# Kernel optimization log

Measured on AMD Instinct MI355X. Metric: run time of the kernel, lower is better.

The kernel has to match this reference:

```python
import jax, jax.numpy as jnp
import numpy as np

K = 10

def _lrelu(v):
    return jax.nn.leaky_relu(v, negative_slope=0.2)

def _knn_idx(x, k):
    # x: [B, C, N]; returns indices of k nearest neighbors [B, N, k]
    xx = jnp.sum(x * x, axis=1, keepdims=True)          # [B,1,N]
    inner = -2.0 * jnp.einsum('bcn,bcm->bnm', x, x)     # [B,N,N]
    pd = -xx - inner - jnp.swapaxes(xx, 1, 2)           # -squared distance [B,N,N]
    _, idx = jax.lax.top_k(pd, k)
    return idx

def _graph_feature(x, k):
    # x: [B, C, N] -> edge features [B, 2C, N, k]
    idx = _knn_idx(x, k)                                # [B,N,k]
    xt = jnp.swapaxes(x, 1, 2)                          # [B,N,C]
    feat = jax.vmap(lambda xb, ib: xb[ib])(xt, idx)     # [B,N,k,C] gather
    center = xt[:, :, None, :]                          # [B,N,1,C]
    f = jnp.concatenate([feat - center,
                         jnp.broadcast_to(center, feat.shape)], axis=-1)  # [B,N,k,2C]
    return jnp.transpose(f, (0, 3, 1, 2))               # [B,2C,N,k]

def _edge_block(x, W, k):
    # conv2d 1x1 (no bias) + LeakyReLU + max over neighbors
    g = _graph_feature(x, k)                            # [B,2C,N,k]
    h = _lrelu(jnp.einsum('oc,bcnk->bonk', W, g))
    return jnp.max(h, axis=-1)                          # [B,O,N]

def setup_inputs() -> dict:
    key = jax.random.key(0)
    ks = jax.random.split(key, 9)
    def w(k_, *shape):
        fan_in = shape[-1]
        return jax.random.normal(k_, shape, dtype=jnp.float32) / np.sqrt(fan_in)
    return {
        'x':  jax.random.normal(ks[0], (8, 3, 2048), dtype=jnp.float32),
        'W1': w(ks[1], 64, 6),
        'W2': w(ks[2], 64, 128),
        'W3': w(ks[3], 128, 128),
        'W4': w(ks[4], 256, 256),
        'W5': w(ks[5], 512, 512),
        'L1': w(ks[6], 512, 1024),
        'L2': w(ks[7], 256, 512),
        'b2': jnp.zeros((256,), dtype=jnp.float32),
    }

def reference(x, W1, W2, W3, W4, W5, L1, L2, b2):
    x1 = _edge_block(x,  W1, K)   # [B,64,N]
    x2 = _edge_block(x1, W2, K)   # [B,64,N]
    x3 = _edge_block(x2, W3, K)   # [B,128,N]
    x4 = _edge_block(x3, W4, K)   # [B,256,N]
    h = jnp.concatenate([x1, x2, x3, x4], axis=1)        # [B,512,N]
    h = _lrelu(jnp.einsum('oc,bcn->bon', W5, h))         # [B,512,N]
    hmax = jnp.max(h, axis=-1)                           # [B,512]
    havg = jnp.mean(h, axis=-1)                          # [B,512]
    f = jnp.concatenate([hmax, havg], axis=1)            # [B,1024]
    f = _lrelu(f @ L1.T)                                 # [B,512]
    out = _lrelu(f @ L2.T + b2)                          # [B,256]
    return out
```

## Files before the change

kernel.cpp:

```cpp
#include <hip/hip_runtime.h>
#include <cstdint>
#include <cstddef>

constexpr int B_ = 8;
constexpr int N_ = 2048;
constexpr int K_ = 10;

typedef __attribute__((ext_vector_type(8))) short bf16x8;
typedef __attribute__((ext_vector_type(4))) float f32x4;

__device__ __forceinline__ float lrelu(float v) { return fmaxf(v, 0.2f * v); }

__device__ __forceinline__ short f2bf(float f) {
    uint32_t u = __builtin_bit_cast(uint32_t, f);
    u += 0x7fff + ((u >> 16) & 1);
    return (short)(u >> 16);
}

__global__ void k_transpose(const float* __restrict__ x, float* __restrict__ xt) {
    int i = blockIdx.x * 256 + threadIdx.x;
    if (i >= B_ * N_) return;
    int b = i / N_, n = i % N_;
#pragma unroll
    for (int c = 0; c < 3; ++c)
        xt[(size_t)i * 3 + c] = x[((size_t)b * 3 + c) * N_ + n];
}

__global__ void k_cvt(const float* __restrict__ W4, const float* __restrict__ W5,
                      short* __restrict__ Wb4, short* __restrict__ W5b) {
    int i = blockIdx.x * 256 + threadIdx.x;
    if (i < 256 * 128) {
        Wb4[i] = f2bf(W4[(size_t)(i >> 7) * 256 + (i & 127)]);
    } else {
        int k = i - 256 * 128;
        if (k < 512 * 512) W5b[k] = f2bf(W5[k]);
    }
}

__global__ void k_norms(const float* __restrict__ xt, int LD, int OFF, int C,
                        float* __restrict__ nrm) {
    int gid = blockIdx.x * 256 + threadIdx.x;
    int wid = gid >> 6;
    int lane = threadIdx.x & 63;
    if (wid >= B_ * N_) return;
    const float* row = xt + (size_t)wid * LD + OFF;
    float s = 0.f;
    for (int c = lane; c < C; c += 64) { float v = row[c]; s += v * v; }
#pragma unroll
    for (int off = 32; off; off >>= 1) s += __shfl_down(s, off);
    if (lane == 0) nrm[wid] = s;
}

__global__ __launch_bounds__(256) void k_knn3(const float* __restrict__ x,
                                              int* __restrict__ idxout) {
    __shared__ float xs[3][N_];
    __shared__ float ns[N_];
    const int b = blockIdx.x;
    const int w = threadIdx.x >> 6, lane = threadIdx.x & 63;
    const int n = blockIdx.y * 4 + w;
    for (int e = threadIdx.x; e < 3 * N_; e += 256)
        xs[e / N_][e % N_] = x[(size_t)b * 3 * N_ + e];
    __syncthreads();
    for (int m = threadIdx.x; m < N_; m += 256) {
        float a0 = xs[0][m], a1 = xs[1][m], a2 = xs[2][m];
        ns[m] = a0 * a0 + a1 * a1 + a2 * a2;
    }
    __syncthreads();
    const float q0 = xs[0][n], q1 = xs[1][n], q2 = xs[2][n];

    float sv[32];
#pragma unroll
    for (int g = 0; g < 32; ++g) {
        int m = g * 64 + lane;
        sv[g] = 2.f * (q0 * xs[0][m] + q1 * xs[1][m] + q2 * xs[2][m]) - ns[m];
    }
    float lm = sv[0];
#pragma unroll
    for (int g = 1; g < 32; ++g) lm = fmaxf(lm, sv[g]);
    float cur = lm, T = lm;
#pragma unroll
    for (int i = 0; i < K_; ++i) {
        float wm = cur;
#pragma unroll
        for (int off = 1; off < 64; off <<= 1) wm = fmaxf(wm, __shfl_xor(wm, off));
        T = wm;
        unsigned long long m = __ballot(cur == wm);
        int first = __ffsll(m) - 1;
        if (lane == first) cur = -INFINITY;
    }
    float kv[K_]; int ki[K_];
#pragma unroll
    for (int i = 0; i < K_; ++i) { kv[i] = -INFINITY; ki[i] = 0x7fffffff; }
#pragma unroll
    for (int g = 0; g < 32; ++g) {
        unsigned long long mk = __ballot(sv[g] >= T && sv[g] > kv[0]);
        while (mk) {
            int l = __ffsll(mk) - 1;
            mk &= mk - 1;
            float v = __shfl(sv[g], l);
            if (v > kv[0]) {
                kv[0] = v; ki[0] = g * 64 + l;
#pragma unroll
                for (int u = 0; u < K_ - 1; ++u)
                    if (kv[u] > kv[u + 1]) {
                        float tv = kv[u]; kv[u] = kv[u + 1]; kv[u + 1] = tv;
                        int tix = ki[u]; ki[u] = ki[u + 1]; ki[u + 1] = tix;
                    }
            }
        }
    }
    if (lane == 0) {
        int* op = idxout + ((size_t)b * N_ + n) * K_;
#pragma unroll
        for (int k = 0; k < K_; ++k) op[k] = ki[K_ - 1 - k];
    }
}

template <int C>
__global__ __launch_bounds__(256) void k_scores(const float* __restrict__ xt, int LD, int OFF,
                                                const float* __restrict__ nrm,
                                                float* __restrict__ S, int b0) {
    constexpr int KC = 32;
    constexpr int T = N_ / 64;
    __shared__ __align__(16) float XN[64][36];
    __shared__ __align__(16) float XM[64][36];
    __shared__ __align__(16) float TT[16][68];
    const int bl = blockIdx.x;
    const int b = b0 + bl;
    int p = blockIdx.y;
    int r = 0, off = 0;
    while (off + (T - r) <= p) { off += T - r; ++r; }
    const int ti = r, tj = r + (p - off);
    const int n0 = ti * 64, m0 = tj * 64;
    const int t = threadIdx.x;
    const int tn = t & 15, to = t >> 4;
    const float* xb = xt + ((size_t)b * N_) * LD + OFF;
    const float* nb = nrm + (size_t)b * N_;
    float* Sb = S + (size_t)bl * N_ * N_;

    float acc[4][4];
#pragma unroll
    for (int i = 0; i < 4; ++i)
#pragma unroll
        for (int j = 0; j < 4; ++j) acc[i][j] = 0.f;

    for (int c0 = 0; c0 < C; c0 += KC) {
        __syncthreads();
        for (int e = t; e < 64 * (KC / 4); e += 256) {
            int rr = e >> 3, g = e & 7;
            *(float4*)&XN[rr][g * 4] =
                *(const float4*)&xb[(size_t)(n0 + rr) * LD + c0 + g * 4];
            *(float4*)&XM[rr][g * 4] =
                *(const float4*)&xb[(size_t)(m0 + rr) * LD + c0 + g * 4];
        }
        __syncthreads();
#pragma unroll
        for (int c4 = 0; c4 < KC / 4; ++c4) {
            float4 xn[4], xm[4];
#pragma unroll
            for (int i = 0; i < 4; ++i) xn[i] = *(const float4*)&XN[tn + 16 * i][c4 * 4];
#pragma unroll
            for (int j = 0; j < 4; ++j) xm[j] = *(const float4*)&XM[to * 4 + j][c4 * 4];
#pragma unroll
            for (int i = 0; i < 4; ++i)
#pragma unroll
                for (int j = 0; j < 4; ++j)
                    acc[i][j] += xn[i].x * xm[j].x + xn[i].y * xm[j].y +
                                 xn[i].z * xm[j].z + xn[i].w * xm[j].w;
        }
    }

    float nm[4];
#pragma unroll
    for (int j = 0; j < 4; ++j) nm[j] = nb[m0 + to * 4 + j];
#pragma unroll
    for (int pp = 0; pp < 4; ++pp) {
        __syncthreads();
#pragma unroll
        for (int j = 0; j < 4; ++j) TT[tn][to * 4 + j] = 2.f * acc[pp][j] - nm[j];
        __syncthreads();
        f32x4 vv = *(const f32x4*)&TT[to][tn * 4];
        __builtin_nontemporal_store(vv, (f32x4*)&Sb[(size_t)(n0 + pp * 16 + to) * N_ + m0 + tn * 4]);
    }

    if (ti != tj) {
        float nn[4];
#pragma unroll
        for (int i = 0; i < 4; ++i) nn[i] = nb[n0 + tn + 16 * i];
#pragma unroll
        for (int pp = 0; pp < 4; ++pp) {
            __syncthreads();
            if ((to >> 2) == pp) {
                int tq = (to & 3) * 4;
#pragma unroll
                for (int j = 0; j < 4; ++j)
#pragma unroll
                    for (int i = 0; i < 4; ++i)
                        TT[tq + j][tn + 16 * i] = 2.f * acc[i][j] - nn[i];
            }
            __syncthreads();
            f32x4 vv = *(const f32x4*)&TT[to][tn * 4];
            __builtin_nontemporal_store(vv, (f32x4*)&Sb[(size_t)(m0 + pp * 16 + to) * N_ + n0 + tn * 4]);
        }
    }
}

__global__ __launch_bounds__(256) void k_topk(const float* __restrict__ S,
                                              int* __restrict__ idxout, int b0) {
    const int bl = blockIdx.x, b = b0 + bl;
    const int wv = threadIdx.x >> 6, lane = threadIdx.x & 63;
    const int n = blockIdx.y * 4 + wv;
    const float* row = S + (size_t)bl * N_ * N_ + (size_t)n * N_;

    float sv[32];
#pragma unroll
    for (int g = 0; g < 32; ++g) sv[g] = __builtin_nontemporal_load(&row[g * 64 + lane]);

    float lm = sv[0];
#pragma unroll
    for (int g = 1; g < 32; ++g) lm = fmaxf(lm, sv[g]);

    float cur = lm, T = lm;
#pragma unroll
    for (int i = 0; i < K_; ++i) {
        float wm = cur;
#pragma unroll
        for (int off = 1; off < 64; off <<= 1) wm = fmaxf(wm, __shfl_xor(wm, off));
        T = wm;
        unsigned long long m = __ballot(cur == wm);
        int first = __ffsll(m) - 1;
        if (lane == first) cur = -INFINITY;
    }

    float kv[K_]; int ki[K_];
#pragma unroll
    for (int i = 0; i < K_; ++i) { kv[i] = -INFINITY; ki[i] = 0x7fffffff; }

#pragma unroll
    for (int g = 0; g < 32; ++g) {
        unsigned long long mk = __ballot(sv[g] >= T && sv[g] > kv[0]);
        while (mk) {
            int l = __ffsll(mk) - 1;
            mk &= mk - 1;
            float v = __shfl(sv[g], l);
            if (v > kv[0]) {
                kv[0] = v; ki[0] = g * 64 + l;
#pragma unroll
                for (int u = 0; u < K_ - 1; ++u)
                    if (kv[u] > kv[u + 1]) {
                        float tv = kv[u]; kv[u] = kv[u + 1]; kv[u + 1] = tv;
                        int tix = ki[u]; ki[u] = ki[u + 1]; ki[u + 1] = tix;
                    }
            }
        }
    }
    if (lane == 0) {
        int* op = idxout + ((size_t)b * N_ + n) * K_;
#pragma unroll
        for (int k = 0; k < K_; ++k) op[k] = ki[K_ - 1 - k];
    }
}

template <int C, int O>
__global__ __launch_bounds__(256) void k_center(const float* __restrict__ xt, int LD, int OFF,
                                                const float* __restrict__ W,
                                                float* __restrict__ tbuf) {
    constexpr int KC = (C == 3) ? 4 : 32;
    __shared__ __align__(16) float XT[64][36];
    __shared__ __align__(16) float WDT[KC][68];
    const int b = blockIdx.x;
    const int n0 = blockIdx.y * 64;
    const int ob = blockIdx.z * 64;
    const int t = threadIdx.x;
    const int tn = t & 15, to = t >> 4;
    const float* xb = xt + ((size_t)b * N_) * LD + OFF;
    float4 acc[4];
#pragma unroll
    for (int i = 0; i < 4; ++i) acc[i] = make_float4(0, 0, 0, 0);
    for (int c0 = 0; c0 < C; c0 += KC) {
        __syncthreads();
        for (int e = t; e < 64 * KC; e += 256) {
            int r = e / KC, cc = e % KC;
            XT[r][cc] = (C == 3) ? ((cc < 3) ? xb[(size_t)(n0 + r) * LD + cc] : 0.f)
                                 : xb[(size_t)(n0 + r) * LD + c0 + cc];
        }
        for (int e = t; e < 64 * KC; e += 256) {
            int oo = e / KC, cc = e % KC;
            float wd, wc;
            if (C == 3) {
                wd = (cc < 3) ? W[(ob + oo) * 6 + cc] : 0.f;
                wc = (cc < 3) ? W[(ob + oo) * 6 + 3 + cc] : 0.f;
            } else {
                wd = W[(size_t)(ob + oo) * (2 * C) + c0 + cc];
                wc = W[(size_t)(ob + oo) * (2 * C) + C + c0 + cc];
            }
            WDT[cc][oo] = wc - wd;
        }
        __syncthreads();
#pragma unroll 4
        for (int cc = 0; cc < KC; ++cc) {
            float4 w4 = *(const float4*)&WDT[cc][to * 4];
#pragma unroll
            for (int i = 0; i < 4; ++i) {
                float a = XT[tn * 4 + i][cc];
                acc[i].x += a * w4.x; acc[i].y += a * w4.y;
                acc[i].z += a * w4.z; acc[i].w += a * w4.w;
            }
        }
    }
#pragma unroll
    for (int i = 0; i < 4; ++i)
        *(float4*)&tbuf[((size_t)b * N_ + n0 + tn * 4 + i) * O + ob + to * 4] = acc[i];
}

template <int C, int O>
__global__ __launch_bounds__(256) void k_conv(const float* __restrict__ xt, int LDI, int OFFI,
                                              const int* __restrict__ idx,
                                              const float* __restrict__ W,
                                              const float* __restrict__ tbuf,
                                              float* __restrict__ hout, int OFFO) {
    constexpr int KC = (C == 3) ? 4 : 32;
    __shared__ __align__(16) float A[160][36];
    __shared__ __align__(16) float WT[KC][68];
    __shared__ int nb_s[160];
    const int b = blockIdx.x;
    const int n0 = blockIdx.y * 16;
    const int t = threadIdx.x;
    const int p = t >> 4, og = t & 15;
    if (t < 160) nb_s[t] = idx[((size_t)b * N_ + n0 + t / K_) * K_ + (t % K_)];
    const float* xb = xt + ((size_t)b * N_) * LDI + OFFI;

    for (int ob = 0; ob < O; ob += 64) {
        float4 acc[K_];
#pragma unroll
        for (int j = 0; j < K_; ++j) acc[j] = make_float4(0, 0, 0, 0);
        for (int c0 = 0; c0 < C; c0 += KC) {
            __syncthreads();
            if (C == 3) {
                for (int e = t; e < 160 * 4; e += 256) {
                    int r = e / 4, cc = e % 4;
                    A[r][cc] = (cc < 3) ? xb[(size_t)nb_s[r] * LDI + cc] : 0.f;
                }
            } else {
                for (int e = t; e < 160 * 8; e += 256) {
                    int r = e / 8, c4 = e % 8;
                    *(float4*)&A[r][c4 * 4] =
                        *(const float4*)&xb[(size_t)nb_s[r] * LDI + c0 + c4 * 4];
                }
            }
            for (int e = t; e < 64 * KC; e += 256) {
                int oo = e / KC, cc = e % KC;
                float w;
                if (C == 3) w = (cc < 3) ? W[(ob + oo) * 6 + cc] : 0.f;
                else        w = W[(size_t)(ob + oo) * (2 * C) + c0 + cc];
                WT[cc][oo] = w;
            }
            __syncthreads();
#pragma unroll 4
            for (int cc = 0; cc < KC; ++cc) {
                float4 w4 = *(const float4*)&WT[cc][og * 4];
#pragma unroll
                for (int j = 0; j < K_; ++j) {
                    float a = A[p * K_ + j][cc];
                    acc[j].x += a * w4.x; acc[j].y += a * w4.y;
                    acc[j].z += a * w4.z; acc[j].w += a * w4.w;
                }
            }
        }
        float4 tv = *(const float4*)&tbuf[((size_t)b * N_ + n0 + p) * O + ob + og * 4];
        float4 mx = acc[0];
#pragma unroll
        for (int j = 1; j < K_; ++j) {
            mx.x = fmaxf(mx.x, acc[j].x); mx.y = fmaxf(mx.y, acc[j].y);
            mx.z = fmaxf(mx.z, acc[j].z); mx.w = fmaxf(mx.w, acc[j].w);
        }
        float4 r;
        r.x = lrelu(mx.x + tv.x); r.y = lrelu(mx.y + tv.y);
        r.z = lrelu(mx.z + tv.z); r.w = lrelu(mx.w + tv.w);
        *(float4*)&hout[((size_t)b * N_ + n0 + p) * 512 + OFFO + ob + og * 4] = r;
    }
}

__global__ __launch_bounds__(256) void k_conv4_mfma(const float* __restrict__ hcat,
                                                    const int* __restrict__ idx,
                                                    const short* __restrict__ Wb,
                                                    const float* __restrict__ tbuf,
                                                    float* __restrict__ hout) {
    __shared__ short Ab[160 * 128];
    __shared__ int nb_s[160];
    const int b = blockIdx.x;
    const int n0 = blockIdx.y * 16;
    const int t = threadIdx.x;
    const int lane = t & 63, wv = t >> 6;
    const int colg = lane & 15, kg = lane >> 4;
    if (t < 160) nb_s[t] = idx[((size_t)b * N_ + n0 + t / K_) * K_ + (t % K_)];
    __syncthreads();
    for (int e = t; e < 160 * 32; e += 256) {
        int r = e >> 5, q = e & 31;
        const float4 v = *(const float4*)&hcat[((size_t)b * N_ + nb_s[r]) * 512 + 128 + q * 4];
        short4 s4 = { f2bf(v.x), f2bf(v.y), f2bf(v.z), f2bf(v.w) };
        int byte = r * 256 + ((q * 8) ^ (((r / K_) & 7) << 4));
        *(short4*)((char*)Ab + byte) = s4;
    }
    bf16x8 bf[4][4];
    const int ob = wv * 64;
#pragma unroll
    for (int nt = 0; nt < 4; ++nt)
#pragma unroll
        for (int ks = 0; ks < 4; ++ks)
            bf[nt][ks] = *(const bf16x8*)&Wb[(size_t)(ob + nt * 16 + colg) * 128 + ks * 32 + kg * 8];
    __syncthreads();

    f32x4 macc[4];
#pragma unroll
    for (int nt = 0; nt < 4; ++nt)
        macc[nt] = (f32x4){-INFINITY, -INFINITY, -INFINITY, -INFINITY};

    const int arow = colg * K_;
    const int aswz = (colg & 7) << 4;
#pragma unroll
    for (int j = 0; j < K_; ++j) {
        f32x4 acc[4];
#pragma unroll
        for (int nt = 0; nt < 4; ++nt) acc[nt] = (f32x4){0.f, 0.f, 0.f, 0.f};
#pragma unroll
        for (int ks = 0; ks < 4; ++ks) {
            int byte = (arow + j) * 256 + (((ks * 32 + kg * 8) * 2) ^ aswz);
            bf16x8 af = *(const bf16x8*)((const char*)Ab + byte);
#pragma unroll
            for (int nt = 0; nt < 4; ++nt)
                acc[nt] = __builtin_amdgcn_mfma_f32_16x16x32_bf16(af, bf[nt][ks], acc[nt], 0, 0, 0);
        }
#pragma unroll
        for (int nt = 0; nt < 4; ++nt) {
            macc[nt].x = fmaxf(macc[nt].x, acc[nt].x);
            macc[nt].y = fmaxf(macc[nt].y, acc[nt].y);
            macc[nt].z = fmaxf(macc[nt].z, acc[nt].z);
            macc[nt].w = fmaxf(macc[nt].w, acc[nt].w);
        }
    }
#pragma unroll
    for (int nt = 0; nt < 4; ++nt)
#pragma unroll
        for (int r = 0; r < 4; ++r) {
            int p = kg * 4 + r;
            int o = ob + nt * 16 + colg;
            float v = macc[nt][r] + tbuf[((size_t)b * N_ + n0 + p) * 256 + o];
            hout[((size_t)b * N_ + n0 + p) * 512 + 256 + o] = lrelu(v);
        }
}

__global__ __launch_bounds__(256) void k_final_mfma(const float* __restrict__ hcat,
                                                    const short* __restrict__ W5b,
                                                    float* __restrict__ pmax,
                                                    float* __restrict__ psum) {
    __shared__ short Ab[64 * 128];
    const int b = blockIdx.x, nc = blockIdx.y, obk = blockIdx.z;
    const int n0 = nc * 64, ob = obk * 64;
    const int t = threadIdx.x, lane = t & 63, wv = t >> 6;
    const int colg = lane & 15, kg = lane >> 4;
    const int o = ob + wv * 16 + colg;

    f32x4 acc[4];
#pragma unroll
    for (int mt = 0; mt < 4; ++mt) acc[mt] = (f32x4){0.f, 0.f, 0.f, 0.f};

    for (int kc = 0; kc < 4; ++kc) {
        __syncthreads();
        for (int e = t; e < 64 * 32; e += 256) {
            int r = e >> 5, q = e & 31;
            const float4 v = *(const float4*)&hcat[((size_t)b * N_ + n0 + r) * 512 + kc * 128 + q * 4];
            short4 s4 = { f2bf(v.x), f2bf(v.y), f2bf(v.z), f2bf(v.w) };
            int byte = r * 256 + ((q * 8) ^ ((r & 7) << 4));
            *(short4*)((char*)Ab + byte) = s4;
        }
        __syncthreads();
#pragma unroll
        for (int ks = 0; ks < 4; ++ks) {
            bf16x8 bfrag = *(const bf16x8*)&W5b[(size_t)o * 512 + kc * 128 + ks * 32 + kg * 8];
#pragma unroll
            for (int mt = 0; mt < 4; ++mt) {
                int row = mt * 16 + colg;
                int byte = row * 256 + (((ks * 32 + kg * 8) * 2) ^ ((row & 7) << 4));
                bf16x8 af = *(const bf16x8*)((const char*)Ab + byte);
                acc[mt] = __builtin_amdgcn_mfma_f32_16x16x32_bf16(af, bfrag, acc[mt], 0, 0, 0);
            }
        }
    }
    float mx = -INFINITY, sm = 0.f;
#pragma unroll
    for (int mt = 0; mt < 4; ++mt)
#pragma unroll
        for (int r = 0; r < 4; ++r) {
            float v = lrelu(acc[mt][r]);
            mx = fmaxf(mx, v); sm += v;
        }
    mx = fmaxf(mx, __shfl_xor(mx, 16)); sm += __shfl_xor(sm, 16);
    mx = fmaxf(mx, __shfl_xor(mx, 32)); sm += __shfl_xor(sm, 32);
    if (lane < 16) {
        pmax[((size_t)b * 512 + ob + wv * 16 + lane) * 32 + nc] = mx;
        psum[((size_t)b * 512 + ob + wv * 16 + lane) * 32 + nc] = sm;
    }
}

__global__ __launch_bounds__(256) void k_pool(const float* __restrict__ pmax,
                                              const float* __restrict__ psum,
                                              float* __restrict__ f) {
    int i = blockIdx.x * 256 + threadIdx.x;
    if (i >= B_ * 512) return;
    int b = i >> 9, o = i & 511;
    const float* pm = pmax + (size_t)i * 32;
    const float* ps = psum + (size_t)i * 32;
    float mm = -INFINITY, ss = 0.f;
#pragma unroll
    for (int q = 0; q < 32; ++q) { mm = fmaxf(mm, pm[q]); ss += ps[q]; }
    f[(size_t)b * 1024 + o] = mm;
    f[(size_t)b * 1024 + 512 + o] = ss * (1.0f / 2048.0f);
}

__global__ __launch_bounds__(256) void k_fc1(const float* __restrict__ f,
                                             const float* __restrict__ L1,
                                             float* __restrict__ f1) {
    __shared__ float fs[8][1024];
    const int t = threadIdx.x, lane = t & 63, w = t >> 6;
    for (int e = t; e < 2048; e += 256)
        *(float4*)&fs[0][e * 4] = *(const float4*)&f[e * 4];
    __syncthreads();
    const int o = blockIdx.x * 4 + w;
    float acc[8];
#pragma unroll
    for (int b = 0; b < 8; ++b) acc[b] = 0.f;
    const float* Lrow = L1 + (size_t)o * 1024;
#pragma unroll
    for (int e = 0; e < 16; ++e) {
        float wv = Lrow[e * 64 + lane];
#pragma unroll
        for (int b = 0; b < 8; ++b) acc[b] += wv * fs[b][e * 64 + lane];
    }
#pragma unroll
    for (int off = 32; off; off >>= 1)
#pragma unroll
        for (int b = 0; b < 8; ++b) acc[b] += __shfl_xor(acc[b], off);
#pragma unroll
    for (int b = 0; b < 8; ++b)
        if (lane == b) f1[(size_t)b * 512 + o] = lrelu(acc[b]);
}

__global__ __launch_bounds__(256) void k_fc2(const float* __restrict__ f1,
                                             const float* __restrict__ L2,
                                             const float* __restrict__ b2,
                                             float* __restrict__ out) {
    __shared__ float fs[8][512];
    const int t = threadIdx.x, lane = t & 63, w = t >> 6;
    for (int e = t; e < 1024; e += 256)
        *(float4*)&fs[0][e * 4] = *(const float4*)&f1[e * 4];
    __syncthreads();
    const int o = blockIdx.x * 4 + w;
    float acc[8];
#pragma unroll
    for (int b = 0; b < 8; ++b) acc[b] = 0.f;
    const float* Lrow = L2 + (size_t)o * 512;
#pragma unroll
    for (int e = 0; e < 8; ++e) {
        float wv = Lrow[e * 64 + lane];
#pragma unroll
        for (int b = 0; b < 8; ++b) acc[b] += wv * fs[b][e * 64 + lane];
    }
#pragma unroll
    for (int off = 32; off; off >>= 1)
#pragma unroll
        for (int b = 0; b < 8; ++b) acc[b] += __shfl_xor(acc[b], off);
    float bb = b2[o];
#pragma unroll
    for (int b = 0; b < 8; ++b)
        if (lane == b) out[(size_t)b * 256 + o] = lrelu(acc[b] + bb);
}

extern "C" void kernel_launch(void* const* d_in, const int* in_sizes, int n_in,
                              void* d_out, int out_size, void* d_ws, size_t ws_size,
                              hipStream_t stream) {
    (void)in_sizes; (void)n_in; (void)out_size;
    const float* x  = (const float*)d_in[0];
    const float* W1 = (const float*)d_in[1];
    const float* W2 = (const float*)d_in[2];
    const float* W3 = (const float*)d_in[3];
    const float* W4 = (const float*)d_in[4];
    const float* W5 = (const float*)d_in[5];
    const float* L1 = (const float*)d_in[6];
    const float* L2 = (const float*)d_in[7];
    const float* b2 = (const float*)d_in[8];
    float* out = (float*)d_out;

    float* ws   = (float*)d_ws;
    float* xt   = ws;
    float* nrm  = xt + (size_t)B_ * N_ * 3;
    int*   idxb = (int*)(nrm + (size_t)B_ * N_);
    float* tb   = (float*)(idxb + (size_t)B_ * N_ * K_);
    float* hcat = tb + (size_t)B_ * N_ * 256;
    float* pmax = hcat + (size_t)B_ * N_ * 512;
    float* psum = pmax + (size_t)B_ * 512 * 32;
    short* wb4  = (short*)(psum + (size_t)B_ * 512 * 32);
    short* w5b  = wb4 + 256 * 128;
    float* fbuf = (float*)(w5b + 512 * 512);
    float* f1b  = fbuf + 8192;
    float* scor = f1b + 4096;

    const size_t base_f = 49152 + 16384 + 163840 + 4194304 + 8388608 +
                          131072 + 131072 + 16384 + 131072 + 8192 + 4096;
    const size_t nsq = (size_t)N_ * N_;
    size_t avail = (ws_size / 4 > base_f) ? (ws_size / 4 - base_f) : 0;
    int CH = 1;
    if (avail >= 8 * nsq) CH = 8;
    else if (avail >= 4 * nsq) CH = 4;
    else if (avail >= 2 * nsq) CH = 2;

    constexpr int TP = (N_ / 64) * (N_ / 64 + 1) / 2;

    dim3 blk(256);
    k_transpose<<<dim3((B_ * N_ + 255) / 256), blk, 0, stream>>>(x, xt);
    k_cvt<<<dim3((256 * 128 + 512 * 512 + 255) / 256), blk, 0, stream>>>(W4, W5, wb4, w5b);

    k_knn3<<<dim3(B_, N_ / 4), blk, 0, stream>>>(x, idxb);
    k_center<3, 64><<<dim3(B_, N_ / 64, 1), blk, 0, stream>>>(xt, 3, 0, W1, tb);
    k_conv<3, 64><<<dim3(B_, N_ / 16), blk, 0, stream>>>(xt, 3, 0, idxb, W1, tb, hcat, 0);

    k_norms<<<dim3(B_ * N_ / 4), blk, 0, stream>>>(hcat, 512, 0, 64, nrm);
    for (int b0 = 0; b0 < B_; b0 += CH) {
        k_scores<64><<<dim3(CH, TP), blk, 0, stream>>>(hcat, 512, 0, nrm, scor, b0);
        k_topk<<<dim3(CH, N_ / 4), blk, 0, stream>>>(scor, idxb, b0);
    }
    k_center<64, 64><<<dim3(B_, N_ / 64, 1), blk, 0, stream>>>(hcat, 512, 0, W2, tb);
    k_conv<64, 64><<<dim3(B_, N_ / 16), blk, 0, stream>>>(hcat, 512, 0, idxb, W2, tb, hcat, 64);

    k_norms<<<dim3(B_ * N_ / 4), blk, 0, stream>>>(hcat, 512, 64, 64, nrm);
    for (int b0 = 0; b0 < B_; b0 += CH) {
        k_scores<64><<<dim3(CH, TP), blk, 0, stream>>>(hcat, 512, 64, nrm, scor, b0);
        k_topk<<<dim3(CH, N_ / 4), blk, 0, stream>>>(scor, idxb, b0);
    }
    k_center<64, 128><<<dim3(B_, N_ / 64, 2), blk, 0, stream>>>(hcat, 512, 64, W3, tb);
    k_conv<64, 128><<<dim3(B_, N_ / 16), blk, 0, stream>>>(hcat, 512, 64, idxb, W3, tb, hcat, 128);

    k_norms<<<dim3(B_ * N_ / 4), blk, 0, stream>>>(hcat, 512, 128, 128, nrm);
    for (int b0 = 0; b0 < B_; b0 += CH) {
        k_scores<128><<<dim3(CH, TP), blk, 0, stream>>>(hcat, 512, 128, nrm, scor, b0);
        k_topk<<<dim3(CH, N_ / 4), blk, 0, stream>>>(scor, idxb, b0);
    }
    k_center<128, 256><<<dim3(B_, N_ / 64, 4), blk, 0, stream>>>(hcat, 512, 128, W4, tb);
    k_conv4_mfma<<<dim3(B_, N_ / 16), blk, 0, stream>>>(hcat, idxb, wb4, tb, hcat);

    k_final_mfma<<<dim3(B_, 32, 8), blk, 0, stream>>>(hcat, w5b, pmax, psum);
    k_pool<<<dim3(B_ * 512 / 256), blk, 0, stream>>>(pmax, psum, fbuf);
    k_fc1<<<dim3(128), blk, 0, stream>>>(fbuf, L1, f1b);
    k_fc2<<<dim3(64), blk, 0, stream>>>(f1b, L2, b2, out);
}
```

Baseline: 558.2 us.

## Store kNN score matrix in bf16 and rescore top candidates exactly in fp32

The score kernel now writes the N×N pairwise score matrix as bf16 instead of fp32, halving the write and read traffic of the large intermediate. The top-k kernel reads the bf16 rows and finds a conservative threshold from the bf16 top-10. It then recomputes exact fp32 dot-product scores from hcat for every candidate at or above that threshold and selects the final indices from those. Less memory also lets more batches fit per chunk. The cost is extra wave-wide reductions and gathers per candidate, and bf16 ties can enlarge the candidate set. There is also a small risk of missing neighbours whose bf16 rounding falls below the threshold.

```diff
diff --git a/kernel.cpp b/kernel.cpp
--- a/kernel.cpp
+++ b/kernel.cpp
@@ -8,6 +8,7 @@
 
 typedef __attribute__((ext_vector_type(8))) short bf16x8;
 typedef __attribute__((ext_vector_type(4))) float f32x4;
+typedef __attribute__((ext_vector_type(4))) short s16x4;
 
 __device__ __forceinline__ float lrelu(float v) { return fmaxf(v, 0.2f * v); }
 
@@ -15,6 +16,10 @@
     uint32_t u = __builtin_bit_cast(uint32_t, f);
     u += 0x7fff + ((u >> 16) & 1);
     return (short)(u >> 16);
+}
+__device__ __forceinline__ float bf2f(unsigned short u) {
+    uint32_t x = ((uint32_t)u) << 16;
+    return __builtin_bit_cast(float, x);
 }
 
 __global__ void k_transpose(const float* __restrict__ x, float* __restrict__ xt) {
@@ -119,7 +124,7 @@
 template <int C>
 __global__ __launch_bounds__(256) void k_scores(const float* __restrict__ xt, int LD, int OFF,
                                                 const float* __restrict__ nrm,
-                                                float* __restrict__ S, int b0) {
+                                                unsigned short* __restrict__ S, int b0) {
     constexpr int KC = 32;
     constexpr int T = N_ / 64;
     __shared__ __align__(16) float XN[64][36];
@@ -136,7 +141,7 @@
     const int tn = t & 15, to = t >> 4;
     const float* xb = xt + ((size_t)b * N_) * LD + OFF;
     const float* nb = nrm + (size_t)b * N_;
-    float* Sb = S + (size_t)bl * N_ * N_;
+    unsigned short* Sb = S + (size_t)bl * N_ * N_;
 
     float acc[4][4];
 #pragma unroll
@@ -179,8 +184,9 @@
 #pragma unroll
         for (int j = 0; j < 4; ++j) TT[tn][to * 4 + j] = 2.f * acc[pp][j] - nm[j];
         __syncthreads();
-        f32x4 vv = *(const f32x4*)&TT[to][tn * 4];
-        __builtin_nontemporal_store(vv, (f32x4*)&Sb[(size_t)(n0 + pp * 16 + to) * N_ + m0 + tn * 4]);
+        float4 vv = *(const float4*)&TT[to][tn * 4];
+        s16x4 sv = { f2bf(vv.x), f2bf(vv.y), f2bf(vv.z), f2bf(vv.w) };
+        __builtin_nontemporal_store(sv, (s16x4*)&Sb[(size_t)(n0 + pp * 16 + to) * N_ + m0 + tn * 4]);
     }
 
     if (ti != tj) {
@@ -199,27 +205,37 @@
                         TT[tq + j][tn + 16 * i] = 2.f * acc[i][j] - nn[i];
             }
             __syncthreads();
-            f32x4 vv = *(const f32x4*)&TT[to][tn * 4];
-            __builtin_nontemporal_store(vv, (f32x4*)&Sb[(size_t)(m0 + pp * 16 + to) * N_ + n0 + tn * 4]);
-        }
-    }
-}
-
-__global__ __launch_bounds__(256) void k_topk(const float* __restrict__ S,
+            float4 vv = *(const float4*)&TT[to][tn * 4];
+            s16x4 sv = { f2bf(vv.x), f2bf(vv.y), f2bf(vv.z), f2bf(vv.w) };
+            __builtin_nontemporal_store(sv, (s16x4*)&Sb[(size_t)(m0 + pp * 16 + to) * N_ + n0 + tn * 4]);
+        }
+    }
+}
+
+template <int C>
+__global__ __launch_bounds__(256) void k_topk(const unsigned short* __restrict__ S,
+                                              const float* __restrict__ hcat, int LD, int OFF,
+                                              const float* __restrict__ nrm,
                                               int* __restrict__ idxout, int b0) {
     const int bl = blockIdx.x, b = b0 + bl;
     const int wv = threadIdx.x >> 6, lane = threadIdx.x & 63;
     const int n = blockIdx.y * 4 + wv;
-    const float* row = S + (size_t)bl * N_ * N_ + (size_t)n * N_;
-
-    float sv[32];
-#pragma unroll
-    for (int g = 0; g < 32; ++g) sv[g] = __builtin_nontemporal_load(&row[g * 64 + lane]);
-
-    float lm = sv[0];
-#pragma unroll
-    for (int g = 1; g < 32; ++g) lm = fmaxf(lm, sv[g]);
-
+    const unsigned short* row = S + (size_t)bl * N_ * N_ + (size_t)n * N_;
+
+    float sv[8][4];
+#pragma unroll
+    for (int g = 0; g < 8; ++g) {
+        uint2 u = *(const uint2*)&row[g * 256 + lane * 4];
+        sv[g][0] = bf2f((unsigned short)(u.x & 0xffffu));
+        sv[g][1] = bf2f((unsigned short)(u.x >> 16));
+        sv[g][2] = bf2f((unsigned short)(u.y & 0xffffu));
+        sv[g][3] = bf2f((unsigned short)(u.y >> 16));
+    }
+    float lm = sv[0][0];
+#pragma unroll
+    for (int g = 0; g < 8; ++g)
+#pragma unroll
+        for (int e = 0; e < 4; ++e) lm = fmaxf(lm, sv[g][e]);
     float cur = lm, T = lm;
 #pragma unroll
     for (int i = 0; i < K_; ++i) {
@@ -231,33 +247,77 @@
         int first = __ffsll(m) - 1;
         if (lane == first) cur = -INFINITY;
     }
-
-    float kv[K_]; int ki[K_];
-#pragma unroll
-    for (int i = 0; i < K_; ++i) { kv[i] = -INFINITY; ki[i] = 0x7fffffff; }
-
-#pragma unroll
-    for (int g = 0; g < 32; ++g) {
-        unsigned long long mk = __ballot(sv[g] >= T && sv[g] > kv[0]);
+    float kv[K_];
+#pragma unroll
+    for (int i = 0; i < K_; ++i) kv[i] = -INFINITY;
+#pragma unroll
+    for (int g = 0; g < 8; ++g) {
+        float m4 = fmaxf(fmaxf(sv[g][0], sv[g][1]), fmaxf(sv[g][2], sv[g][3]));
+        unsigned long long mk = __ballot(m4 >= T && m4 > kv[0]);
         while (mk) {
             int l = __ffsll(mk) - 1;
             mk &= mk - 1;
-            float v = __shfl(sv[g], l);
-            if (v > kv[0]) {
-                kv[0] = v; ki[0] = g * 64 + l;
-#pragma unroll
-                for (int u = 0; u < K_ - 1; ++u)
-                    if (kv[u] > kv[u + 1]) {
-                        float tv = kv[u]; kv[u] = kv[u + 1]; kv[u + 1] = tv;
-                        int tix = ki[u]; ki[u] = ki[u + 1]; ki[u + 1] = tix;
+            float v0 = __shfl(sv[g][0], l), v1 = __shfl(sv[g][1], l);
+            float v2 = __shfl(sv[g][2], l), v3 = __shfl(sv[g][3], l);
+            float vb[4] = {v0, v1, v2, v3};
+#pragma unroll
+            for (int e = 0; e < 4; ++e) {
+                float v = vb[e];
+                if (v >= T && v > kv[0]) {
+                    kv[0] = v;
+#pragma unroll
+                    for (int u = 0; u < K_ - 1; ++u)
+                        if (kv[u] > kv[u + 1]) { float tv = kv[u]; kv[u] = kv[u + 1]; kv[u + 1] = tv; }
+                }
+            }
+        }
+    }
+    const float Tb10 = kv[0];
+    const float* hq = hcat + ((size_t)b * N_ + n) * LD + OFF;
+    float xq0 = hq[lane];
+    float xq1 = (C == 128) ? hq[64 + lane] : 0.f;
+    const float* nb = nrm + (size_t)b * N_;
+    float kv2[K_]; int ki2[K_];
+#pragma unroll
+    for (int i = 0; i < K_; ++i) { kv2[i] = -INFINITY; ki2[i] = 0x7fffffff; }
+#pragma unroll
+    for (int g = 0; g < 8; ++g) {
+        float m4 = fmaxf(fmaxf(sv[g][0], sv[g][1]), fmaxf(sv[g][2], sv[g][3]));
+        unsigned long long mk = __ballot(m4 >= Tb10);
+        while (mk) {
+            int l = __ffsll(mk) - 1;
+            mk &= mk - 1;
+            float v0 = __shfl(sv[g][0], l), v1 = __shfl(sv[g][1], l);
+            float v2 = __shfl(sv[g][2], l), v3 = __shfl(sv[g][3], l);
+            float vb[4] = {v0, v1, v2, v3};
+            const int base = g * 256 + l * 4;
+#pragma unroll
+            for (int e = 0; e < 4; ++e) {
+                if (vb[e] >= Tb10) {
+                    int m = base + e;
+                    const float* hm = hcat + ((size_t)b * N_ + m) * LD + OFF;
+                    float pr = xq0 * hm[lane];
+                    if (C == 128) pr += xq1 * hm[64 + lane];
+#pragma unroll
+                    for (int off = 1; off < 64; off <<= 1) pr += __shfl_xor(pr, off);
+                    float s = 2.f * pr - nb[m];
+                    if (s > kv2[0]) {
+                        kv2[0] = s; ki2[0] = m;
+#pragma unroll
+                        for (int u = 0; u < K_ - 1; ++u)
+                            if (kv2[u] > kv2[u + 1]) {
+                                float tv = kv2[u]; kv2[u] = kv2[u + 1]; kv2[u + 1] = tv;
+                                int ti2 = ki2[u]; ki2[u] = ki2[u + 1]; ki2[u + 1] = ti2;
+                            }
                     }
+                }
             }
         }
     }
     if (lane == 0) {
         int* op = idxout + ((size_t)b * N_ + n) * K_;
 #pragma unroll
-        for (int k = 0; k < K_; ++k) op[k] = ki[K_ - 1 - k];
+        for (int k = 0; k < K_; ++k) op[k] = ki2[K_ - 1 - k];
     }
 }
 
@@ -603,16 +663,16 @@
     short* w5b  = wb4 + 256 * 128;
     float* fbuf = (float*)(w5b + 512 * 512);
     float* f1b  = fbuf + 8192;
-    float* scor = f1b + 4096;
+    unsigned short* scor = (unsigned short*)(f1b + 4096);
 
     const size_t base_f = 49152 + 16384 + 163840 + 4194304 + 8388608 +
                           131072 + 131072 + 16384 + 131072 + 8192 + 4096;
     const size_t nsq = (size_t)N_ * N_;
     size_t avail = (ws_size / 4 > base_f) ? (ws_size / 4 - base_f) : 0;
     int CH = 1;
-    if (avail >= 8 * nsq) CH = 8;
-    else if (avail >= 4 * nsq) CH = 4;
-    else if (avail >= 2 * nsq) CH = 2;
+    if (avail >= 8 * nsq / 2) CH = 8;
+    else if (avail >= 4 * nsq / 2) CH = 4;
+    else if (avail >= 2 * nsq / 2) CH = 2;
 
     constexpr int TP = (N_ / 64) * (N_ / 64 + 1) / 2;
 
@@ -627,7 +687,7 @@
     k_norms<<<dim3(B_ * N_ / 4), blk, 0, stream>>>(hcat, 512, 0, 64, nrm);
     for (int b0 = 0; b0 < B_; b0 += CH) {
         k_scores<64><<<dim3(CH, TP), blk, 0, stream>>>(hcat, 512, 0, nrm, scor, b0);
-        k_topk<<<dim3(CH, N_ / 4), blk, 0, stream>>>(scor, idxb, b0);
+        k_topk<64><<<dim3(CH, N_ / 4), blk, 0, stream>>>(scor, hcat, 512, 0, nrm, idxb, b0);
     }
     k_center<64, 64><<<dim3(B_, N_ / 64, 1), blk, 0, stream>>>(hcat, 512, 0, W2, tb);
     k_conv<64, 64><<<dim3(B_, N_ / 16), blk, 0, stream>>>(hcat, 512, 0, idxb, W2, tb, hcat, 64);
@@ -635,7 +695,7 @@
     k_norms<<<dim3(B_ * N_ / 4), blk, 0, stream>>>(hcat, 512, 64, 64, nrm);
     for (int b0 = 0; b0 < B_; b0 += CH) {
         k_scores<64><<<dim3(CH, TP), blk, 0, stream>>>(hcat, 512, 64, nrm, scor, b0);
-        k_topk<<<dim3(CH, N_ / 4), blk, 0, stream>>>(scor, idxb, b0);
+        k_topk<64><<<dim3(CH, N_ / 4), blk, 0, stream>>>(scor, hcat, 512, 64, nrm, idxb, b0);
     }
     k_center<64, 128><<<dim3(B_, N_ / 64, 2), blk, 0, stream>>>(hcat, 512, 64, W3, tb);
     k_conv<64, 128><<<dim3(B_, N_ / 16), blk, 0, stream>>>(hcat, 512, 64, idxb, W3, tb, hcat, 128);
@@ -643,7 +703,7 @@
     k_norms<<<dim3(B_ * N_ / 4), blk, 0, stream>>>(hcat, 512, 128, 128, nrm);
     for (int b0 = 0; b0 < B_; b0 += CH) {
         k_scores<128><<<dim3(CH, TP), blk, 0, stream>>>(hcat, 512, 128, nrm, scor, b0);
-        k_topk<<<dim3(CH, N_ / 4), blk, 0, stream>>>(scor, idxb, b0);
+        k_topk<128><<<dim3(CH, N_ / 4), blk, 0, stream>>>(scor, hcat, 512, 128, nrm, idxb, b0);
     }
     k_center<128, 256><<<dim3(B_, N_ / 64, 4), blk, 0, stream>>>(hcat, 512, 128, W4, tb);
     k_conv4_mfma<<<dim3(B_, N_ / 16), blk, 0, stream>>>(hcat, idxb, wb4, tb, hcat);
```

Measured after the change: 652.1 us. 16.8% more time.

## Compute kNN pairwise scores with split-bf16 MFMA instead of FP32 FMA

Applied to the files above, without the earlier changes.

Replaces the FP32 scalar Gram-matrix kernel for kNN scores with an MFMA bf16 kernel. It uses a three-pass hi/lo bf16 split (hi*hi + lo*hi + hi*lo) to approximate FP32 accuracy, and stores the staged tiles in swizzled LDS. The epilogue now writes scores directly from the accumulator fragments, including the transposed mirror tile, in place of the LDS-transposed nontemporal vector stores. This trades cheaper matrix math for extra conversion work and less coalesced stores. The dropped lo*lo term may also change neighbor selection on near-ties.

```diff
diff --git a/kernel.cpp b/kernel.cpp
--- a/kernel.cpp
+++ b/kernel.cpp
@@ -15,6 +15,10 @@
     uint32_t u = __builtin_bit_cast(uint32_t, f);
     u += 0x7fff + ((u >> 16) & 1);
     return (short)(u >> 16);
+}
+__device__ __forceinline__ float bf2f(short s) {
+    uint32_t x = ((uint32_t)(unsigned short)s) << 16;
+    return __builtin_bit_cast(float, x);
 }
 
 __global__ void k_transpose(const float* __restrict__ x, float* __restrict__ xt) {
@@ -117,90 +121,89 @@
 }
 
 template <int C>
-__global__ __launch_bounds__(256) void k_scores(const float* __restrict__ xt, int LD, int OFF,
-                                                const float* __restrict__ nrm,
-                                                float* __restrict__ S, int b0) {
-    constexpr int KC = 32;
+__global__ __launch_bounds__(256) void k_scores_mfma(const float* __restrict__ xt, int LD, int OFF,
+                                                     const float* __restrict__ nrm,
+                                                     float* __restrict__ S, int b0) {
+    constexpr int RPC = C / 64;
+    constexpr int NCH = 3 * RPC;
     constexpr int T = N_ / 64;
-    __shared__ __align__(16) float XN[64][36];
-    __shared__ __align__(16) float XM[64][36];
-    __shared__ __align__(16) float TT[16][68];
+    __shared__ short AN[64 * 64];
+    __shared__ short AM[64 * 64];
     const int bl = blockIdx.x;
     const int b = b0 + bl;
     int p = blockIdx.y;
-    int r = 0, off = 0;
-    while (off + (T - r) <= p) { off += T - r; ++r; }
-    const int ti = r, tj = r + (p - off);
+    int r0 = 0, off = 0;
+    while (off + (T - r0) <= p) { off += T - r0; ++r0; }
+    const int ti = r0, tj = r0 + (p - off);
     const int n0 = ti * 64, m0 = tj * 64;
     const int t = threadIdx.x;
-    const int tn = t & 15, to = t >> 4;
+    const int lane = t & 63, w = t >> 6;
+    const int colg = lane & 15, kg = lane >> 4;
     const float* xb = xt + ((size_t)b * N_) * LD + OFF;
     const float* nb = nrm + (size_t)b * N_;
     float* Sb = S + (size_t)bl * N_ * N_;
 
-    float acc[4][4];
-#pragma unroll
-    for (int i = 0; i < 4; ++i)
-#pragma unroll
-        for (int j = 0; j < 4; ++j) acc[i][j] = 0.f;
-
-    for (int c0 = 0; c0 < C; c0 += KC) {
+    f32x4 acc[4];
+#pragma unroll
+    for (int j = 0; j < 4; ++j) acc[j] = (f32x4){0.f, 0.f, 0.f, 0.f};
+
+    for (int ch = 0; ch < NCH; ++ch) {
+        const int region = ch / RPC;
+        const int cc0 = (ch % RPC) * 64;
         __syncthreads();
-        for (int e = t; e < 64 * (KC / 4); e += 256) {
-            int rr = e >> 3, g = e & 7;
-            *(float4*)&XN[rr][g * 4] =
-                *(const float4*)&xb[(size_t)(n0 + rr) * LD + c0 + g * 4];
-            *(float4*)&XM[rr][g * 4] =
-                *(const float4*)&xb[(size_t)(m0 + rr) * LD + c0 + g * 4];
+#pragma unroll
+        for (int e = 0; e < 4; ++e) {
+            int idx = t + e * 256;
+            int r = idx >> 4, q = idx & 15;
+            float4 vn = *(const float4*)&xb[(size_t)(n0 + r) * LD + cc0 + q * 4];
+            float4 vm = *(const float4*)&xb[(size_t)(m0 + r) * LD + cc0 + q * 4];
+            float an4[4] = {vn.x, vn.y, vn.z, vn.w};
+            float am4[4] = {vm.x, vm.y, vm.z, vm.w};
+            short sa[4], sb[4];
+#pragma unroll
+            for (int c2 = 0; c2 < 4; ++c2) {
+                short hn = f2bf(an4[c2]);
+                short hm = f2bf(am4[c2]);
+                sa[c2] = (region == 1) ? f2bf(an4[c2] - bf2f(hn)) : hn;
+                sb[c2] = (region == 2) ? f2bf(am4[c2] - bf2f(hm)) : hm;
+            }
+            int base16 = r * 128 + (q >> 1) * 16;
+            int byte = (base16 ^ ((r & 7) << 4)) + (q & 1) * 8;
+            *(short4*)((char*)AN + byte) = make_short4(sa[0], sa[1], sa[2], sa[3]);
+            *(short4*)((char*)AM + byte) = make_short4(sb[0], sb[1], sb[2], sb[3]);
         }
         __syncthreads();
-#pragma unroll
-        for (int c4 = 0; c4 < KC / 4; ++c4) {
-            float4 xn[4], xm[4];
-#pragma unroll
-            for (int i = 0; i < 4; ++i) xn[i] = *(const float4*)&XN[tn + 16 * i][c4 * 4];
-#pragma unroll
-            for (int j = 0; j < 4; ++j) xm[j] = *(const float4*)&XM[to * 4 + j][c4 * 4];
-#pragma unroll
-            for (int i = 0; i < 4; ++i)
-#pragma unroll
-                for (int j = 0; j < 4; ++j)
-                    acc[i][j] += xn[i].x * xm[j].x + xn[i].y * xm[j].y +
-                                 xn[i].z * xm[j].z + xn[i].w * xm[j].w;
-        }
-    }
-
-    float nm[4];
-#pragma unroll
-    for (int j = 0; j < 4; ++j) nm[j] = nb[m0 + to * 4 + j];
-#pragma unroll
-    for (int pp = 0; pp < 4; ++pp) {
-        __syncthreads();
-#pragma unroll
-        for (int j = 0; j < 4; ++j) TT[tn][to * 4 + j] = 2.f * acc[pp][j] - nm[j];
-        __syncthreads();
-        f32x4 vv = *(const f32x4*)&TT[to][tn * 4];
-        __builtin_nontemporal_store(vv, (f32x4*)&Sb[(size_t)(n0 + pp * 16 + to) * N_ + m0 + tn * 4]);
-    }
-
+        const int arow = w * 16 + colg;
+#pragma unroll
+        for (int s = 0; s < 2; ++s) {
+            int abyte = (arow * 128 + s * 64 + kg * 16) ^ ((arow & 7) << 4);
+            bf16x8 af = *(const bf16x8*)((const char*)AN + abyte);
+#pragma unroll
+            for (int j = 0; j < 4; ++j) {
+                int brow = j * 16 + colg;
+                int bbyte = (brow * 128 + s * 64 + kg * 16) ^ ((brow & 7) << 4);
+                bf16x8 bfr = *(const bf16x8*)((const char*)AM + bbyte);
+                acc[j] = __builtin_amdgcn_mfma_f32_16x16x32_bf16(af, bfr, acc[j], 0, 0, 0);
+            }
+        }
+    }
+#pragma unroll
+    for (int j = 0; j < 4; ++j) {
+        float nm = nb[m0 + j * 16 + colg];
+#pragma unroll
+        for (int r = 0; r < 4; ++r) {
+            int row = n0 + w * 16 + kg * 4 + r;
+            Sb[(size_t)row * N_ + m0 + j * 16 + colg] = 2.f * acc[j][r] - nm;
+        }
+    }
     if (ti != tj) {
-        float nn[4];
-#pragma unroll
-        for (int i = 0; i < 4; ++i) nn[i] = nb[n0 + tn + 16 * i];
-#pragma unroll
-        for (int pp = 0; pp < 4; ++pp) {
-            __syncthreads();
-            if ((to >> 2) == pp) {
-                int tq = (to & 3) * 4;
-#pragma unroll
-                for (int j = 0; j < 4; ++j)
-#pragma unroll
-                    for (int i = 0; i < 4; ++i)
-                        TT[tq + j][tn + 16 * i] = 2.f * acc[i][j] - nn[i];
-            }
-            __syncthreads();
-            f32x4 vv = *(const f32x4*)&TT[to][tn * 4];
-            __builtin_nontemporal_store(vv, (f32x4*)&Sb[(size_t)(m0 + pp * 16 + to) * N_ + n0 + tn * 4]);
+#pragma unroll
+        for (int r = 0; r < 4; ++r) {
+            int nrow = n0 + w * 16 + kg * 4 + r;
+            float nn = nb[nrow];
+#pragma unroll
+            for (int j = 0; j < 4; ++j)
+                Sb[(size_t)(m0 + j * 16 + colg) * N_ + nrow] = 2.f * acc[j][r] - nn;
         }
     }
 }
@@ -626,7 +629,7 @@
 
     k_norms<<<dim3(B_ * N_ / 4), blk, 0, stream>>>(hcat, 512, 0, 64, nrm);
     for (int b0 = 0; b0 < B_; b0 += CH) {
-        k_scores<64><<<dim3(CH, TP), blk, 0, stream>>>(hcat, 512, 0, nrm, scor, b0);
+        k_scores_mfma<64><<<dim3(CH, TP), blk, 0, stream>>>(hcat, 512, 0, nrm, scor, b0);
         k_topk<<<dim3(CH, N_ / 4), blk, 0, stream>>>(scor, idxb, b0);
     }
     k_center<64, 64><<<dim3(B_, N_ / 64, 1), blk, 0, stream>>>(hcat, 512, 0, W2, tb);
@@ -634,7 +637,7 @@
 
     k_norms<<<dim3(B_ * N_ / 4), blk, 0, stream>>>(hcat, 512, 64, 64, nrm);
     for (int b0 = 0; b0 < B_; b0 += CH) {
-        k_scores<64><<<dim3(CH, TP), blk, 0, stream>>>(hcat, 512, 64, nrm, scor, b0);
+        k_scores_mfma<64><<<dim3(CH, TP), blk, 0, stream>>>(hcat, 512, 64, nrm, scor, b0);
         k_topk<<<dim3(CH, N_ / 4), blk, 0, stream>>>(scor, idxb, b0);
     }
     k_center<64, 128><<<dim3(B_, N_ / 64, 2), blk, 0, stream>>>(hcat, 512, 64, W3, tb);
@@ -642,7 +645,7 @@
 
     k_norms<<<dim3(B_ * N_ / 4), blk, 0, stream>>>(hcat, 512, 128, 128, nrm);
     for (int b0 = 0; b0 < B_; b0 += CH) {
-        k_scores<128><<<dim3(CH, TP), blk, 0, stream>>>(hcat, 512, 128, nrm, scor, b0);
+        k_scores_mfma<128><<<dim3(CH, TP), blk, 0, stream>>>(hcat, 512, 128, nrm, scor, b0);
         k_topk<<<dim3(CH, N_ / 4), blk, 0, stream>>>(scor, idxb, b0);
     }
     k_center<128, 256><<<dim3(B_, N_ / 64, 4), blk, 0, stream>>>(hcat, 512, 128, W4, tb);
```

Measured after the change: 544.9 us. 2.4% less time.
